# Kernel tuning notes

Hardware: AMD Instinct MI355X
Metric: run time of the kernel (lower is better)

Reference implementation:

```python
import jax, jax.numpy as jnp
import numpy as np

D = 1024       # d_model
H = 16         # num_heads
HD = D // H    # head_dim = 64
CS = 1024      # chunk_size
GS = 256       # global_context_size
CR = 4         # compression_ratio -> num_summary = CS // CR = 256
B = 2
S = 4096       # seq_len -> 4 chunks, no padding
NUM_CHUNKS = S // CS
SCALE = 1.0 / np.sqrt(HD)


def setup_inputs() -> dict:
    key = jax.random.key(0)
    ks = jax.random.split(key, 16)

    def lin(k, din, dout):
        kw, kb = jax.random.split(k)
        w = jax.random.normal(kw, (din, dout), jnp.float32) * (1.0 / np.sqrt(din))
        b = jnp.zeros((dout,), jnp.float32)
        return w, b

    cq_w, cq_b = lin(ks[0], D, D)
    ck_w, ck_b = lin(ks[1], D, D)
    cv_w, cv_b = lin(ks[2], D, D)
    co_w, co_b = lin(ks[3], D, D)
    qkv_w, qkv_b = lin(ks[4], D, 3 * D)
    lo_w, lo_b = lin(ks[5], D, D)
    summary_queries = jax.random.truncated_normal(ks[6], -2.0, 2.0, (1, CS // CR, D), jnp.float32) * 0.02
    x = jax.random.normal(ks[7], (B, S, D), jnp.float32)
    return {
        "x": x, "summary_queries": summary_queries,
        "cq_w": cq_w, "cq_b": cq_b, "ck_w": ck_w, "ck_b": ck_b,
        "cv_w": cv_w, "cv_b": cv_b, "co_w": co_w, "co_b": co_b,
        "qkv_w": qkv_w, "qkv_b": qkv_b, "lo_w": lo_w, "lo_b": lo_b,
    }


def _heads(t):
    # [B, L, D] -> [B, H, L, HD]
    b, l, _ = t.shape
    return jnp.transpose(t.reshape(b, l, H, HD), (0, 2, 1, 3))


def _unheads(t):
    # [B, H, L, HD] -> [B, L, D]
    b, _, l, _ = t.shape
    return jnp.transpose(t, (0, 2, 1, 3)).reshape(b, l, D)


def _compress_chunk(chunk, summary_queries, cq_w, cq_b, ck_w, ck_b, cv_w, cv_b, co_w, co_b):
    # chunk: [B, CS, D] -> [B, CS//CR, D] via learned-query cross-attention
    bsz = chunk.shape[0]
    sq = jnp.broadcast_to(summary_queries, (bsz, summary_queries.shape[1], D))
    q = _heads(sq @ cq_w + cq_b)        # [B, H, Ns, HD]
    k = _heads(chunk @ ck_w + ck_b)     # [B, H, CS, HD]
    v = _heads(chunk @ cv_w + cv_b)
    scores = jnp.einsum('bhqd,bhkd->bhqk', q, k) * SCALE
    weights = jax.nn.softmax(scores, axis=-1)
    out = _unheads(jnp.einsum('bhqk,bhkd->bhqd', weights, v))
    return out @ co_w + co_b


def _local_attention(chunk, gctx, qkv_w, qkv_b, lo_w, lo_b):
    # chunk: [B, CS, D], gctx: [B, G, D]
    g = gctx.shape[1]
    combined = jnp.concatenate([gctx, chunk], axis=1)   # [B, G+CS, D]
    cl = combined.shape[1]
    qkv = combined @ qkv_w + qkv_b
    q, k, v = jnp.split(qkv, 3, axis=-1)
    q, k, v = _heads(q), _heads(k), _heads(v)
    scores = jnp.einsum('bhqd,bhkd->bhqk', q, k) * SCALE
    # full visibility to global tokens, causal elsewhere
    idx = jnp.arange(cl)
    mask = (idx[None, :] < g) | (idx[None, :] <= idx[:, None])  # [cl, cl]
    scores = jnp.where(mask[None, None, :, :], scores, -1e9)
    weights = jax.nn.softmax(scores, axis=-1)
    attended = _unheads(jnp.einsum('bhqk,bhkd->bhqd', weights, v))
    attended = attended @ lo_w + lo_b
    return attended[:, g:] + chunk


def reference(x, summary_queries, cq_w, cq_b, ck_w, ck_b, cv_w, cv_b, co_w, co_b,
              qkv_w, qkv_b, lo_w, lo_b):
    comp = lambda c: _compress_chunk(c, summary_queries, cq_w, cq_b, ck_w, ck_b,
                                     cv_w, cv_b, co_w, co_b)
    # num_chunks > 1: global context = compression of first chunk (Ns == GS, no trunc)
    gctx = comp(x[:, :CS])
    outputs = []
    for i in range(NUM_CHUNKS):
        chunk = x[:, i * CS:(i + 1) * CS]
        chunk_out = _local_attention(chunk, gctx, qkv_w, qkv_b, lo_w, lo_b)
        outputs.append(chunk_out)
        if i < NUM_CHUNKS - 1:
            summ = comp(chunk_out)                       # [B, 256, D]
            gctx = jnp.concatenate([gctx, summ], axis=1)[:, -GS:]
    return jnp.concatenate(outputs, axis=1)  # [B, S, D]
```

## Files before the change

kernel.cpp:

```cpp
#include <hip/hip_runtime.h>

using bf16x8 = __attribute__((ext_vector_type(8))) short;
using f32x4  = __attribute__((ext_vector_type(4))) float;
using us4    = __attribute__((ext_vector_type(4))) unsigned short;

static __device__ __forceinline__ unsigned short f2bf(float x) {
  union { float f; unsigned u; } v; v.f = x;
  unsigned r = v.u + 0x7FFFu + ((v.u >> 16) & 1u);
  return (unsigned short)(r >> 16);
}
static __device__ __forceinline__ unsigned pack2bf(float a, float b) {
  return (unsigned)f2bf(a) | ((unsigned)f2bf(b) << 16);
}
static __device__ __forceinline__ void gload16(const unsigned short* g, unsigned short* lds_base) {
  __builtin_amdgcn_global_load_lds(
      (const __attribute__((address_space(1))) unsigned int*)g,
      (__attribute__((address_space(3))) unsigned int*)lds_base, 16, 0, 0);
}

#define SCALE_L2E 0.18033688011112042f
#define M0_L2E    14.426950408889634f

__global__ __launch_bounds__(256) void k_cvt(const float* __restrict__ in,
                                             unsigned short* __restrict__ out, int n4) {
  int i = blockIdx.x * 256 + threadIdx.x;
  if (i >= n4) return;
  float4 v = ((const float4*)in)[i];
  us4 o = { f2bf(v.x), f2bf(v.y), f2bf(v.z), f2bf(v.w) };
  ((us4*)out)[i] = o;
}

__global__ __launch_bounds__(256) void k_twt_all(
    const float* __restrict__ cq, const float* __restrict__ ck, const float* __restrict__ cv,
    const float* __restrict__ lo, const float* __restrict__ qkv,
    unsigned short* __restrict__ wqt, unsigned short* __restrict__ wkvt,
    unsigned short* __restrict__ wlot, unsigned short* __restrict__ wqkvt) {
  __shared__ float tile[32][33];
  int id = blockIdx.x;
  const float* W; unsigned short* Wt; int N;
  if (id < 1024)      { W = cq;  Wt = wqt;                N = 1024; }
  else if (id < 2048) { W = ck;  Wt = wkvt;               N = 1024; id -= 1024; }
  else if (id < 3072) { W = cv;  Wt = wkvt + 1024 * 1024; N = 1024; id -= 2048; }
  else if (id < 4096) { W = lo;  Wt = wlot;               N = 1024; id -= 3072; }
  else                { W = qkv; Wt = wqkvt;              N = 3072; id -= 4096; }
  int ntb = N >> 5;
  int nb = (id % ntb) * 32, kb = (id / ntb) * 32;
  int t = threadIdx.x;
  int k = t >> 3, n4 = (t & 7) << 2;
  float4 v = *(const float4*)&W[(size_t)(kb + k) * N + nb + n4];
  tile[k][n4] = v.x; tile[k][n4 + 1] = v.y; tile[k][n4 + 2] = v.z; tile[k][n4 + 3] = v.w;
  __syncthreads();
  int n = t >> 3, k4 = (t & 7) << 2;
  us4 o = { f2bf(tile[k4][n]), f2bf(tile[k4 + 1][n]), f2bf(tile[k4 + 2][n]), f2bf(tile[k4 + 3][n]) };
  *(us4*)&Wt[(size_t)(nb + n) * 1024 + kb + k4] = o;
}

__global__ __launch_bounds__(256) void k_bias2a(const float* __restrict__ qkv_w,
                                                const float* __restrict__ co_b,
                                                float* __restrict__ part) {
  int nb = blockIdx.x & 7, jb = blockIdx.x >> 3;
  int n = nb * 256 + threadIdx.x;
  float s = 0.f;
  int j0 = jb * 64;
#pragma unroll 4
  for (int j = j0; j < j0 + 64; ++j) s += co_b[j] * qkv_w[(size_t)j * 3072 + 1024 + n];
  part[jb * 2048 + n] = s;
}

__global__ __launch_bounds__(256) void k_bias2b(const float* __restrict__ part,
                                                const float* __restrict__ qkv_b,
                                                const float* __restrict__ ck_b,
                                                const float* __restrict__ cv_b,
                                                float* __restrict__ bias2,
                                                float* __restrict__ kvb,
                                                float* __restrict__ zbias) {
  int id = blockIdx.x, t = threadIdx.x;
  if (id < 8) {
    int n = id * 256 + t;
    float s = qkv_b[1024 + n];
#pragma unroll
    for (int jb = 0; jb < 16; ++jb) s += part[jb * 2048 + n];
    bias2[n] = s;
  } else {
    for (int j = t; j < 1024; j += 256) {
      kvb[j] = ck_b[j]; kvb[1024 + j] = cv_b[j]; zbias[j] = 0.f;
    }
  }
}

template <int BM, int NSTAGE = (BM == 256 ? 2 : 3)>
__global__ __launch_bounds__(BM * 2) void k_gemm(
    const unsigned short* __restrict__ A, long long bsA, int Lr,
    const unsigned short* __restrict__ Bt, const float* __restrict__ bias,
    unsigned short* __restrict__ outb, int Nout,
    unsigned short* __restrict__ outb2,
    unsigned short* __restrict__ outT, int Lv, int vt_col0,
    const float* __restrict__ resx, float* __restrict__ resout,
    unsigned short* __restrict__ rescob, int chunk,
    int N, int K) {
  constexpr int NWAVES = (BM * 2) / 64;
  constexpr int NA = BM / 16;
  constexpr int NINST = NA + 8;
  constexpr int NPW = NINST / NWAVES;
  static_assert(NPW * NWAVES == NINST, "staging split");
  constexpr int STRIDE = (BM + 128) * 32;
  __shared__ unsigned short Ls[NSTAGE * STRIDE];
  const int m0 = blockIdx.x * BM, n0 = blockIdx.y * 128;
  const int t = threadIdx.x, w = t >> 6, l = t & 63;
  const int wr = (BM == 64) ? 0 : (w >> 1);
  const int wc = (BM == 64) ? w : (w & 1);
  const int lg = l >> 4, lq = l & 15;
  const int batch = m0 / Lr, mrow = m0 % Lr;
  const int srow = l >> 2;
  const int scol = (((l & 3) ^ ((l >> 3) & 3)) << 3);
  const unsigned short* gp[NPW];
  int lofs[NPW];
#pragma unroll
  for (int jj = 0; jj < NPW; ++jj) {
    int j = w * NPW + jj;
    if (j < NA) {
      int r = mrow + j * 16 + srow;
      gp[jj] = A + (size_t)batch * (size_t)bsA + (size_t)r * K + scol;
      lofs[jj] = j * 512;
    } else {
      int r = n0 + (j - NA) * 16 + srow;
      gp[jj] = Bt + (size_t)r * K + scol;
      lofs[jj] = BM * 32 + (j - NA) * 512;
    }
  }
  const int lsw = (lg ^ ((lq >> 1) & 3)) * 8;
  const f32x4 fz = {0.f, 0.f, 0.f, 0.f};
  f32x4 acc[4][4];
#pragma unroll
  for (int i = 0; i < 4; ++i)
#pragma unroll
    for (int j = 0; j < 4; ++j) acc[i][j] = fz;
  const int nsteps = K >> 5;
#pragma unroll
  for (int st = 0; st < NSTAGE - 1; ++st) {
    if (st < nsteps) {
#pragma unroll
      for (int jj = 0; jj < NPW; ++jj) gload16(gp[jj] + (st << 5), &Ls[st * STRIDE + lofs[jj]]);
    }
  }
  int cur = 0;
  int nxt = (NSTAGE - 1) * STRIDE;
  for (int s = 0; s < nsteps; ++s) {
    if (s + NSTAGE - 1 < nsteps) {
      const int kk = (s + NSTAGE - 1) << 5;
#pragma unroll
      for (int jj = 0; jj < NPW; ++jj) gload16(gp[jj] + kk, &Ls[nxt + lofs[jj]]);
      asm volatile("s_waitcnt vmcnt(%0)" :: "n"((NSTAGE - 1) * NPW) : "memory");
    } else if (NSTAGE >= 3 && s + 1 < nsteps) {
      asm volatile("s_waitcnt vmcnt(%0)" :: "n"(NPW) : "memory");
    } else {
      asm volatile("s_waitcnt vmcnt(0)" ::: "memory");
    }
    __builtin_amdgcn_s_barrier();
    bf16x8 af[4], bg[4];
#pragma unroll
    for (int i = 0; i < 4; ++i) {
      af[i] = *(const bf16x8*)&Ls[cur + (wr * 64 + i * 16 + lq) * 32 + lsw];
      bg[i] = *(const bf16x8*)&Ls[cur + BM * 32 + (wc * 64 + i * 16 + lq) * 32 + lsw];
    }
#pragma unroll
    for (int i = 0; i < 4; ++i)
#pragma unroll
      for (int j = 0; j < 4; ++j)
        acc[i][j] = __builtin_amdgcn_mfma_f32_16x16x32_bf16(af[i], bg[j], acc[i][j], 0, 0, 0);
    __builtin_amdgcn_s_barrier();
    cur += STRIDE; if (cur == NSTAGE * STRIDE) cur = 0;
    nxt += STRIDE; if (nxt == NSTAGE * STRIDE) nxt = 0;
  }
  const int lr = lg << 2;
#pragma unroll
  for (int i = 0; i < 4; ++i) {
    const int rowb = m0 + wr * 64 + i * 16 + lr;
#pragma unroll
    for (int j = 0; j < 4; ++j) {
      const int col = n0 + wc * 64 + j * 16 + lq;
      const float bv = bias[col];
      float v0 = acc[i][j][0] + bv, v1 = acc[i][j][1] + bv;
      float v2 = acc[i][j][2] + bv, v3 = acc[i][j][3] + bv;
      if (outT && col >= vt_col0) {
        const int vc = col - vt_col0;
        const int hh = vc >> 6, dd = vc & 63;
        const int bb = rowb / Lr, key = rowb % Lr;
        us4 o = { f2bf(v0), f2bf(v1), f2bf(v2), f2bf(v3) };
        *(us4*)&outT[((size_t)((bb << 4) + hh) * 64 + dd) * Lv + key] = o;
      } else if (outb2 && col >= 1024) {
        const int c2 = col - 1024;
        outb2[(size_t)(rowb + 0) * 1024 + c2] = f2bf(v0);
        outb2[(size_t)(rowb + 1) * 1024 + c2] = f2bf(v1);
        outb2[(size_t)(rowb + 2) * 1024 + c2] = f2bf(v2);
        outb2[(size_t)(rowb + 3) * 1024 + c2] = f2bf(v3);
      } else if (resx) {
        const int bb = rowb / Lr, r = rowb % Lr;
        const size_t xo = ((size_t)(bb * 4096 + chunk * 1024 + r)) * 1024 + col;
        const size_t co = ((size_t)(bb * 1024 + r)) * 1024 + col;
        float r0 = v0 + resx[xo];
        float r1 = v1 + resx[xo + 1024];
        float r2 = v2 + resx[xo + 2048];
        float r3 = v3 + resx[xo + 3072];
        resout[xo] = r0; resout[xo + 1024] = r1;
        resout[xo + 2048] = r2; resout[xo + 3072] = r3;
        rescob[co] = f2bf(r0); rescob[co + 1024] = f2bf(r1);
        rescob[co + 2048] = f2bf(r2); rescob[co + 3072] = f2bf(r3);
      } else {
        outb[(size_t)(rowb + 0) * Nout + col] = f2bf(v0);
        outb[(size_t)(rowb + 1) * Nout + col] = f2bf(v1);
        outb[(size_t)(rowb + 2) * Nout + col] = f2bf(v2);
        outb[(size_t)(rowb + 3) * Nout + col] = f2bf(v3);
      }
    }
  }
}

template <int MODE>
__global__ __launch_bounds__(256) void k_fa(
    const unsigned short* __restrict__ Q, long long q_bs, int q_stride, int q_row0,
    const unsigned short* __restrict__ K, long long k_bs, int k_stride,
    const unsigned short* __restrict__ V, int Lk,
    unsigned short* __restrict__ O, int Lq_out,
    float* __restrict__ pl, float* __restrict__ pacc) {
  __shared__ unsigned short Ks[64 * 72];
  __shared__ unsigned short Vs[64 * 72];
  __shared__ unsigned short Ps[4 * 16 * 72];
  const int t = threadIdx.x, w = t >> 6, l = t & 63;
  const int lg = l >> 4, lq = l & 15;
  const int bh = blockIdx.x & 31;
  const int rest = blockIdx.x >> 5;
  const int b = bh >> 4, h = bh & 15;
  int qg, koff, ntiles;
  if (MODE == 1)      { qg = 15 - (rest & 15); koff = (rest >> 4) << 10; ntiles = qg + 1; }
  else if (MODE == 3) { qg = rest & 3;         koff = (rest >> 2) << 8;  ntiles = 4; }
  else                { qg = rest;             koff = 0;                 ntiles = 4; }
  const int qloc = qg * 64 + w * 16 + lq;
  const int qglob = q_row0 + (MODE == 1 ? koff : 0) + qloc;
  const unsigned short* qp = Q + (size_t)b * (size_t)q_bs + (size_t)qglob * q_stride + h * 64;
  bf16x8 qf0 = *(const bf16x8*)&qp[lg * 8];
  bf16x8 qf1 = *(const bf16x8*)&qp[32 + lg * 8];
  const f32x4 fz = {0.f, 0.f, 0.f, 0.f};
  const int pidx = (MODE == 2 ? 0 : (koff << 5)) + bh * (MODE == 3 ? 256 : 1024) + qloc;
  f32x4 acc0, acc1, acc2, acc3;
  float lbase = 0.f;
  if (MODE == 2) {
    lbase = pl[pidx];
    const float* pb = &pacc[(size_t)pidx * 64];
    float4 a0 = *(const float4*)&pb[0 * 16 + lg * 4];
    float4 a1 = *(const float4*)&pb[1 * 16 + lg * 4];
    float4 a2 = *(const float4*)&pb[2 * 16 + lg * 4];
    float4 a3 = *(const float4*)&pb[3 * 16 + lg * 4];
    acc0[0] = a0.x; acc0[1] = a0.y; acc0[2] = a0.z; acc0[3] = a0.w;
    acc1[0] = a1.x; acc1[1] = a1.y; acc1[2] = a1.z; acc1[3] = a1.w;
    acc2[0] = a2.x; acc2[1] = a2.y; acc2[2] = a2.z; acc2[3] = a2.w;
    acc3[0] = a3.x; acc3[1] = a3.y; acc3[2] = a3.z; acc3[3] = a3.w;
  } else {
    acc0 = fz; acc1 = fz; acc2 = fz; acc3 = fz;
  }
  float psum = 0.f;
  const int sr = t >> 2, sc = (t & 3) << 4;
  const unsigned short* kbp = K + (size_t)b * (size_t)k_bs + (size_t)koff * k_stride + h * 64;
  const unsigned short* vbp = V + (size_t)(((b << 4) + h) * 64) * Lk + koff;
  unsigned short* pw = &Ps[(w * 16 + lq) * 72];
  bf16x8 kr0, kr1, vr0, vr1;
  {
    const unsigned short* kp = kbp + (size_t)sr * k_stride + sc;
    kr0 = *(const bf16x8*)kp; kr1 = *(const bf16x8*)(kp + 8);
    const unsigned short* vp = vbp + (size_t)sr * Lk + sc;
    vr0 = *(const bf16x8*)vp; vr1 = *(const bf16x8*)(vp + 8);
  }
#define KFA_SM(Z, KH) do { \
    float e0_ = Z[0] * SCALE_L2E - M0_L2E; \
    float e1_ = Z[1] * SCALE_L2E - M0_L2E; \
    float e2_ = Z[2] * SCALE_L2E - M0_L2E; \
    float e3_ = Z[3] * SCALE_L2E - M0_L2E; \
    if (MODE == 1) { \
      int kg_ = k0 + (KH) * 16 + lg * 4; \
      if (kg_ + 0 > qloc) e0_ = -1e9f; \
      if (kg_ + 1 > qloc) e1_ = -1e9f; \
      if (kg_ + 2 > qloc) e2_ = -1e9f; \
      if (kg_ + 3 > qloc) e3_ = -1e9f; \
    } \
    float p0_ = exp2f(e0_), p1_ = exp2f(e1_), p2_ = exp2f(e2_), p3_ = exp2f(e3_); \
    psum += (p0_ + p1_) + (p2_ + p3_); \
    *(unsigned*)&pw[(KH) * 16 + lg * 4]     = pack2bf(p0_, p1_); \
    *(unsigned*)&pw[(KH) * 16 + lg * 4 + 2] = pack2bf(p2_, p3_); \
  } while (0)
#define KFA_MFMA(A_, B_, C_) __builtin_amdgcn_mfma_f32_16x16x32_bf16(A_, B_, C_, 0, 0, 0)
  for (int kt = 0; kt < ntiles; ++kt) {
    const int k0 = kt * 64;
    __syncthreads();
    *(bf16x8*)&Ks[sr * 72 + sc] = kr0; *(bf16x8*)&Ks[sr * 72 + sc + 8] = kr1;
    *(bf16x8*)&Vs[sr * 72 + sc] = vr0; *(bf16x8*)&Vs[sr * 72 + sc + 8] = vr1;
    __syncthreads();
    if (kt + 1 < ntiles) {
      const unsigned short* kp = kbp + (size_t)(k0 + 64 + sr) * k_stride + sc;
      kr0 = *(const bf16x8*)kp; kr1 = *(const bf16x8*)(kp + 8);
      const unsigned short* vp = vbp + (size_t)sr * Lk + k0 + 64 + sc;
      vr0 = *(const bf16x8*)vp; vr1 = *(const bf16x8*)(vp + 8);
    }
    f32x4 z0 = fz, z1 = fz, z2 = fz, z3 = fz;
    __builtin_amdgcn_s_setprio(1);
    z0 = KFA_MFMA(*(const bf16x8*)&Ks[(0 * 16 + lq) * 72 + lg * 8], qf0, z0);
    z1 = KFA_MFMA(*(const bf16x8*)&Ks[(1 * 16 + lq) * 72 + lg * 8], qf0, z1);
    z2 = KFA_MFMA(*(const bf16x8*)&Ks[(2 * 16 + lq) * 72 + lg * 8], qf0, z2);
    z3 = KFA_MFMA(*(const bf16x8*)&Ks[(3 * 16 + lq) * 72 + lg * 8], qf0, z3);
    z0 = KFA_MFMA(*(const bf16x8*)&Ks[(0 * 16 + lq) * 72 + 32 + lg * 8], qf1, z0);
    z1 = KFA_MFMA(*(const bf16x8*)&Ks[(1 * 16 + lq) * 72 + 32 + lg * 8], qf1, z1);
    z2 = KFA_MFMA(*(const bf16x8*)&Ks[(2 * 16 + lq) * 72 + 32 + lg * 8], qf1, z2);
    z3 = KFA_MFMA(*(const bf16x8*)&Ks[(3 * 16 + lq) * 72 + 32 + lg * 8], qf1, z3);
    __builtin_amdgcn_s_setprio(0);
    KFA_SM(z0, 0); KFA_SM(z1, 1); KFA_SM(z2, 2); KFA_SM(z3, 3);
    asm volatile("s_waitcnt lgkmcnt(0)" ::: "memory");
    __builtin_amdgcn_sched_barrier(0);
    bf16x8 pf0 = *(const bf16x8*)&pw[lg * 8];
    bf16x8 pf1 = *(const bf16x8*)&pw[32 + lg * 8];
    asm volatile("" ::: "memory");
    __builtin_amdgcn_sched_barrier(0);
    __builtin_amdgcn_s_setprio(1);
    acc0 = KFA_MFMA(*(const bf16x8*)&Vs[(0 * 16 + lq) * 72 + lg * 8], pf0, acc0);
    acc1 = KFA_MFMA(*(const bf16x8*)&Vs[(1 * 16 + lq) * 72 + lg * 8], pf0, acc1);
    acc2 = KFA_MFMA(*(const bf16x8*)&Vs[(2 * 16 + lq) * 72 + lg * 8], pf0, acc2);
    acc3 = KFA_MFMA(*(const bf16x8*)&Vs[(3 * 16 + lq) * 72 + lg * 8], pf0, acc3);
    acc0 = KFA_MFMA(*(const bf16x8*)&Vs[(0 * 16 + lq) * 72 + 32 + lg * 8], pf1, acc0);
    acc1 = KFA_MFMA(*(const bf16x8*)&Vs[(1 * 16 + lq) * 72 + 32 + lg * 8], pf1, acc1);
    acc2 = KFA_MFMA(*(const bf16x8*)&Vs[(2 * 16 + lq) * 72 + 32 + lg * 8], pf1, acc2);
    acc3 = KFA_MFMA(*(const bf16x8*)&Vs[(3 * 16 + lq) * 72 + 32 + lg * 8], pf1, acc3);
    __builtin_amdgcn_s_setprio(0);
  }
#undef KFA_SM
#undef KFA_MFMA
  psum += __shfl_xor(psum, 16);
  psum += __shfl_xor(psum, 32);
  if (MODE == 2) {
    float inv = 1.f / (lbase + psum);
    size_t ob = ((size_t)b * Lq_out + qloc) * 1024 + h * 64;
    us4 o0 = { f2bf(acc0[0] * inv), f2bf(acc0[1] * inv), f2bf(acc0[2] * inv), f2bf(acc0[3] * inv) };
    us4 o1 = { f2bf(acc1[0] * inv), f2bf(acc1[1] * inv), f2bf(acc1[2] * inv), f2bf(acc1[3] * inv) };
    us4 o2 = { f2bf(acc2[0] * inv), f2bf(acc2[1] * inv), f2bf(acc2[2] * inv), f2bf(acc2[3] * inv) };
    us4 o3 = { f2bf(acc3[0] * inv), f2bf(acc3[1] * inv), f2bf(acc3[2] * inv), f2bf(acc3[3] * inv) };
    *(us4*)&O[ob + 0 * 16 + lg * 4] = o0;
    *(us4*)&O[ob + 1 * 16 + lg * 4] = o1;
    *(us4*)&O[ob + 2 * 16 + lg * 4] = o2;
    *(us4*)&O[ob + 3 * 16 + lg * 4] = o3;
  } else {
    if (lg == 0) pl[pidx] = psum;
    float* pb = &pacc[(size_t)pidx * 64];
    *(float4*)&pb[0 * 16 + lg * 4] = make_float4(acc0[0], acc0[1], acc0[2], acc0[3]);
    *(float4*)&pb[1 * 16 + lg * 4] = make_float4(acc1[0], acc1[1], acc1[2], acc1[3]);
    *(float4*)&pb[2 * 16 + lg * 4] = make_float4(acc2[0], acc2[1], acc2[2], acc2[3]);
    *(float4*)&pb[3 * 16 + lg * 4] = make_float4(acc3[0], acc3[1], acc3[2], acc3[3]);
  }
}

__global__ __launch_bounds__(256) void k_fam(const float* __restrict__ pl0,
                                             const float* __restrict__ pacc0,
                                             unsigned short* __restrict__ attc) {
  int i = blockIdx.x * 256 + threadIdx.x;
  int row = i >> 4, d4 = (i & 15) << 2;
  float lsum = 0.f;
  float4 o = make_float4(0.f, 0.f, 0.f, 0.f);
#pragma unroll
  for (int s = 0; s < 4; ++s) {
    lsum += pl0[s * 8192 + row];
    float4 a = *(const float4*)&pacc0[((size_t)(s * 8192 + row)) * 64 + d4];
    o.x += a.x; o.y += a.y; o.z += a.z; o.w += a.w;
  }
  float inv = 1.f / lsum;
  int b = row >> 12, h = (row >> 8) & 15, q = row & 255;
  us4 ov = { f2bf(o.x * inv), f2bf(o.y * inv), f2bf(o.z * inv), f2bf(o.w * inv) };
  *(us4*)&attc[((size_t)(b * 256 + q)) * 1024 + h * 64 + d4] = ov;
}

extern "C" void kernel_launch(void* const* d_in, const int* in_sizes, int n_in,
                              void* d_out, int out_size, void* d_ws, size_t ws_size,
                              hipStream_t stream) {
  const float* x     = (const float*)d_in[0];
  const float* sq    = (const float*)d_in[1];
  const float* cq_w  = (const float*)d_in[2];
  const float* cq_b  = (const float*)d_in[3];
  const float* ck_w  = (const float*)d_in[4];
  const float* ck_b  = (const float*)d_in[5];
  const float* cv_w  = (const float*)d_in[6];
  const float* cv_b  = (const float*)d_in[7];
  const float* co_w  = (const float*)d_in[8];
  const float* co_b  = (const float*)d_in[9];
  const float* qkv_w = (const float*)d_in[10];
  const float* qkv_b = (const float*)d_in[11];
  const float* lo_w  = (const float*)d_in[12];
  const float* lo_b  = (const float*)d_in[13];
  float* out = (float*)d_out;

  char* ws = (char*)d_ws;
  size_t off = 0;
  auto alloc = [&](size_t bytes) -> void* {
    void* p = ws + off;
    off += (bytes + 255) & ~(size_t)255;
    return p;
  };
  unsigned short* xb    = (unsigned short*)alloc(16777216);
  unsigned short* sqb   = (unsigned short*)alloc(524288);
  unsigned short* cow16 = (unsigned short*)alloc(2097152);
  unsigned short* wqt   = (unsigned short*)alloc(2097152);
  unsigned short* wkvt  = (unsigned short*)alloc(4194304);
  unsigned short* wlot  = (unsigned short*)alloc(2097152);
  unsigned short* wqkvt = (unsigned short*)alloc(6291456);
  unsigned short* w2t   = (unsigned short*)alloc(4194304);
  float*          bias2 = (float*)alloc(8192);
  float*          kvb   = (float*)alloc(8192);
  float*          zbias = (float*)alloc(4096);
  float*          part  = (float*)alloc(131072);
  unsigned short* qs    = (unsigned short*)alloc(524288);
  unsigned short* qx    = (unsigned short*)alloc(16777216);
  unsigned short* kx    = (unsigned short*)alloc(16777216);
  unsigned short* vtx   = (unsigned short*)alloc(16777216);
  unsigned short* gk    = (unsigned short*)alloc(1048576);
  unsigned short* gvt   = (unsigned short*)alloc(1048576);
  unsigned short* kc    = (unsigned short*)alloc(4194304);
  unsigned short* vtc   = (unsigned short*)alloc(4194304);
  unsigned short* attc  = (unsigned short*)alloc(1048576);
  unsigned short* attl  = (unsigned short*)alloc(4194304);
  unsigned short* cob   = (unsigned short*)alloc(4194304);
  float*          plb   = (float*)alloc(524288);
  float*          pacc  = (float*)alloc(33554432);
  float*          pl0   = (float*)alloc(131072);
  float*          pacc0 = (float*)alloc(8388608);

  k_cvt<<<8192, 256, 0, stream>>>(x, xb, 2097152);
  k_cvt<<<256, 256, 0, stream>>>(sq, sqb, 65536);
  k_cvt<<<1024, 256, 0, stream>>>(co_w, cow16, 262144);
  k_twt_all<<<7168, 256, 0, stream>>>(cq_w, ck_w, cv_w, lo_w, qkv_w, wqt, wkvt, wlot, wqkvt);
  k_bias2a<<<128, 256, 0, stream>>>(qkv_w, co_b, part);
  k_bias2b<<<9, 256, 0, stream>>>(part, qkv_b, ck_b, cv_b, bias2, kvb, zbias);
  k_gemm<64><<<dim3(4, 8), 128, 0, stream>>>(sqb, 0, 256, wqt, cq_b, qs, 1024, nullptr,
                                             nullptr, 0, 0, nullptr, nullptr, nullptr, 0, 1024, 1024);
  k_gemm<128><<<dim3(16, 8), 256, 0, stream>>>(wqkvt + 1024 * 1024, 0, 2048, cow16, zbias,
                                               w2t, 1024, nullptr, nullptr, 0, 0,
                                               nullptr, nullptr, nullptr, 0, 1024, 1024);
  k_gemm<256><<<dim3(32, 24), 512, 0, stream>>>(xb, 4096LL * 1024, 4096, wqkvt, qkv_b,
                                                qx, 1024, kx, vtx, 4096, 2048,
                                                nullptr, nullptr, nullptr, 0, 3072, 1024);
  k_fa<1><<<2048, 256, 0, stream>>>(qx, 4096LL * 1024, 1024, 0,
                                    kx, 4096LL * 1024, 1024,
                                    vtx, 4096, nullptr, 0, plb, pacc);

  auto comp = [&](const unsigned short* inA, long long bsA) {
    k_gemm<64><<<dim3(32, 16), 128, 0, stream>>>(inA, bsA, 1024, wkvt, kvb,
                                                 kc, 1024, nullptr, vtc, 1024, 1024,
                                                 nullptr, nullptr, nullptr, 0, 2048, 1024);
    k_fa<3><<<512, 256, 0, stream>>>(qs, 0LL, 1024, 0,
                                     kc, 1024LL * 1024, 1024,
                                     vtc, 1024, nullptr, 0, pl0, pacc0);
    k_fam<<<512, 256, 0, stream>>>(pl0, pacc0, attc);
    k_gemm<64><<<dim3(8, 16), 128, 0, stream>>>(attc, 256LL * 1024, 256, w2t, bias2,
                                                gk, 1024, nullptr, gvt, 256, 1024,
                                                nullptr, nullptr, nullptr, 0, 2048, 1024);
  };

  comp(xb, 4096LL * 1024);
  for (int i = 0; i < 4; ++i) {
    k_fa<2><<<512, 256, 0, stream>>>(qx, 4096LL * 1024, 1024, i * 1024,
                                     gk, 256LL * 1024, 1024,
                                     gvt, 256, attl, 1024,
                                     plb + (size_t)i * 32768, pacc + (size_t)i * 32768 * 64);
    k_gemm<64><<<dim3(32, 8), 128, 0, stream>>>(attl, 1024LL * 1024, 1024, wlot, lo_b,
                                                nullptr, 1024, nullptr, nullptr, 0, 0,
                                                x, out, cob, i, 1024, 1024);
    if (i < 3) comp(cob, 1024LL * 1024);
  }
}
```

Measured before the change: 477.8 us.

## Drop split-K compression attention, double-buffer FA tiles, fuse conversion kernels

The compression attention no longer splits the 1024 keys into four partial blocks followed by a merge kernel. A new MODE 0 processes all 16 key tiles in a single pass over 128 blocks and writes normalized bf16 output directly. This removes the k_fam launch and the fp32 partial buffers, at the cost of less parallelism per launch. The flash-attention loop now double-buffers the K/V LDS tiles, dropping one __syncthreads per iteration. The three fp32-to-bf16 conversion launches are also merged into one.

```diff
diff --git a/kernel.cpp b/kernel.cpp
--- a/kernel.cpp
+++ b/kernel.cpp
@@ -21,10 +21,17 @@
 #define SCALE_L2E 0.18033688011112042f
 #define M0_L2E    14.426950408889634f
 
-__global__ __launch_bounds__(256) void k_cvt(const float* __restrict__ in,
-                                             unsigned short* __restrict__ out, int n4) {
-  int i = blockIdx.x * 256 + threadIdx.x;
-  if (i >= n4) return;
+__global__ __launch_bounds__(256) void k_cvt3(const float* __restrict__ x,
+                                              const float* __restrict__ sq,
+                                              const float* __restrict__ cw,
+                                              unsigned short* __restrict__ xb,
+                                              unsigned short* __restrict__ sqb,
+                                              unsigned short* __restrict__ cwb) {
+  int id = blockIdx.x;
+  const float* in; unsigned short* out; int i;
+  if (id < 8192)      { in = x;  out = xb;  i = id * 256 + threadIdx.x; }
+  else if (id < 8448) { in = sq; out = sqb; i = (id - 8192) * 256 + threadIdx.x; }
+  else                { in = cw; out = cwb; i = (id - 8448) * 256 + threadIdx.x; }
   float4 v = ((const float4*)in)[i];
   us4 o = { f2bf(v.x), f2bf(v.y), f2bf(v.z), f2bf(v.w) };
   ((us4*)out)[i] = o;
@@ -222,9 +229,9 @@
     const unsigned short* __restrict__ K, long long k_bs, int k_stride,
     const unsigned short* __restrict__ V, int Lk,
     unsigned short* __restrict__ O, int Lq_out,
-    float* __restrict__ pl, float* __restrict__ pacc) {
-  __shared__ unsigned short Ks[64 * 72];
-  __shared__ unsigned short Vs[64 * 72];
+    float* __restrict__ pl, float* __restrict__ pacc, int Lkeys) {
+  __shared__ unsigned short Ks[2][64 * 72];
+  __shared__ unsigned short Vs[2][64 * 72];
   __shared__ unsigned short Ps[4 * 16 * 72];
   const int t = threadIdx.x, w = t >> 6, l = t & 63;
   const int lg = l >> 4, lq = l & 15;
@@ -232,16 +239,15 @@
   const int rest = blockIdx.x >> 5;
   const int b = bh >> 4, h = bh & 15;
   int qg, koff, ntiles;
-  if (MODE == 1)      { qg = 15 - (rest & 15); koff = (rest >> 4) << 10; ntiles = qg + 1; }
-  else if (MODE == 3) { qg = rest & 3;         koff = (rest >> 2) << 8;  ntiles = 4; }
-  else                { qg = rest;             koff = 0;                 ntiles = 4; }
+  if (MODE == 1) { qg = 15 - (rest & 15); koff = (rest >> 4) << 10; ntiles = qg + 1; }
+  else           { qg = rest;             koff = 0;                 ntiles = Lkeys >> 6; }
   const int qloc = qg * 64 + w * 16 + lq;
   const int qglob = q_row0 + (MODE == 1 ? koff : 0) + qloc;
   const unsigned short* qp = Q + (size_t)b * (size_t)q_bs + (size_t)qglob * q_stride + h * 64;
   bf16x8 qf0 = *(const bf16x8*)&qp[lg * 8];
   bf16x8 qf1 = *(const bf16x8*)&qp[32 + lg * 8];
   const f32x4 fz = {0.f, 0.f, 0.f, 0.f};
-  const int pidx = (MODE == 2 ? 0 : (koff << 5)) + bh * (MODE == 3 ? 256 : 1024) + qloc;
+  const int pidx = (MODE == 1 ? (koff << 5) : 0) + bh * 1024 + qloc;
   f32x4 acc0, acc1, acc2, acc3;
   float lbase = 0.f;
   if (MODE == 2) {
@@ -290,9 +296,9 @@
 #define KFA_MFMA(A_, B_, C_) __builtin_amdgcn_mfma_f32_16x16x32_bf16(A_, B_, C_, 0, 0, 0)
   for (int kt = 0; kt < ntiles; ++kt) {
     const int k0 = kt * 64;
-    __syncthreads();
-    *(bf16x8*)&Ks[sr * 72 + sc] = kr0; *(bf16x8*)&Ks[sr * 72 + sc + 8] = kr1;
-    *(bf16x8*)&Vs[sr * 72 + sc] = vr0; *(bf16x8*)&Vs[sr * 72 + sc + 8] = vr1;
+    const int p = kt & 1;
+    *(bf16x8*)&Ks[p][sr * 72 + sc] = kr0; *(bf16x8*)&Ks[p][sr * 72 + sc + 8] = kr1;
+    *(bf16x8*)&Vs[p][sr * 72 + sc] = vr0; *(bf16x8*)&Vs[p][sr * 72 + sc + 8] = vr1;
     __syncthreads();
     if (kt + 1 < ntiles) {
       const unsigned short* kp = kbp + (size_t)(k0 + 64 + sr) * k_stride + sc;
@@ -302,14 +308,14 @@
     }
     f32x4 z0 = fz, z1 = fz, z2 = fz, z3 = fz;
     __builtin_amdgcn_s_setprio(1);
-    z0 = KFA_MFMA(*(const bf16x8*)&Ks[(0 * 16 + lq) * 72 + lg * 8], qf0, z0);
-    z1 = KFA_MFMA(*(const bf16x8*)&Ks[(1 * 16 + lq) * 72 + lg * 8], qf0, z1);
-    z2 = KFA_MFMA(*(const bf16x8*)&Ks[(2 * 16 + lq) * 72 + lg * 8], qf0, z2);
-    z3 = KFA_MFMA(*(const bf16x8*)&Ks[(3 * 16 + lq) * 72 + lg * 8], qf0, z3);
-    z0 = KFA_MFMA(*(const bf16x8*)&Ks[(0 * 16 + lq) * 72 + 32 + lg * 8], qf1, z0);
-    z1 = KFA_MFMA(*(const bf16x8*)&Ks[(1 * 16 + lq) * 72 + 32 + lg * 8], qf1, z1);
-    z2 = KFA_MFMA(*(const bf16x8*)&Ks[(2 * 16 + lq) * 72 + 32 + lg * 8], qf1, z2);
-    z3 = KFA_MFMA(*(const bf16x8*)&Ks[(3 * 16 + lq) * 72 + 32 + lg * 8], qf1, z3);
+    z0 = KFA_MFMA(*(const bf16x8*)&Ks[p][(0 * 16 + lq) * 72 + lg * 8], qf0, z0);
+    z1 = KFA_MFMA(*(const bf16x8*)&Ks[p][(1 * 16 + lq) * 72 + lg * 8], qf0, z1);
+    z2 = KFA_MFMA(*(const bf16x8*)&Ks[p][(2 * 16 + lq) * 72 + lg * 8], qf0, z2);
+    z3 = KFA_MFMA(*(const bf16x8*)&Ks[p][(3 * 16 + lq) * 72 + lg * 8], qf0, z3);
+    z0 = KFA_MFMA(*(const bf16x8*)&Ks[p][(0 * 16 + lq) * 72 + 32 + lg * 8], qf1, z0);
+    z1 = KFA_MFMA(*(const bf16x8*)&Ks[p][(1 * 16 + lq) * 72 + 32 + lg * 8], qf1, z1);
+    z2 = KFA_MFMA(*(const bf16x8*)&Ks[p][(2 * 16 + lq) * 72 + 32 + lg * 8], qf1, z2);
+    z3 = KFA_MFMA(*(const bf16x8*)&Ks[p][(3 * 16 + lq) * 72 + 32 + lg * 8], qf1, z3);
     __builtin_amdgcn_s_setprio(0);
     KFA_SM(z0, 0); KFA_SM(z1, 1); KFA_SM(z2, 2); KFA_SM(z3, 3);
     asm volatile("s_waitcnt lgkmcnt(0)" ::: "memory");
@@ -319,21 +325,28 @@
     asm volatile("" ::: "memory");
     __builtin_amdgcn_sched_barrier(0);
     __builtin_amdgcn_s_setprio(1);
-    acc0 = KFA_MFMA(*(const bf16x8*)&Vs[(0 * 16 + lq) * 72 + lg * 8], pf0, acc0);
-    acc1 = KFA_MFMA(*(const bf16x8*)&Vs[(1 * 16 + lq) * 72 + lg * 8], pf0, acc1);
-    acc2 = KFA_MFMA(*(const bf16x8*)&Vs[(2 * 16 + lq) * 72 + lg * 8], pf0, acc2);
-    acc3 = KFA_MFMA(*(const bf16x8*)&Vs[(3 * 16 + lq) * 72 + lg * 8], pf0, acc3);
-    acc0 = KFA_MFMA(*(const bf16x8*)&Vs[(0 * 16 + lq) * 72 + 32 + lg * 8], pf1, acc0);
-    acc1 = KFA_MFMA(*(const bf16x8*)&Vs[(1 * 16 + lq) * 72 + 32 + lg * 8], pf1, acc1);
-    acc2 = KFA_MFMA(*(const bf16x8*)&Vs[(2 * 16 + lq) * 72 + 32 + lg * 8], pf1, acc2);
-    acc3 = KFA_MFMA(*(const bf16x8*)&Vs[(3 * 16 + lq) * 72 + 32 + lg * 8], pf1, acc3);
+    acc0 = KFA_MFMA(*(const bf16x8*)&Vs[p][(0 * 16 + lq) * 72 + lg * 8], pf0, acc0);
+    acc1 = KFA_MFMA(*(const bf16x8*)&Vs[p][(1 * 16 + lq) * 72 + lg * 8], pf0, acc1);
+    acc2 = KFA_MFMA(*(const bf16x8*)&Vs[p][(2 * 16 + lq) * 72 + lg * 8], pf0, acc2);
+    acc3 = KFA_MFMA(*(const bf16x8*)&Vs[p][(3 * 16 + lq) * 72 + lg * 8], pf0, acc3);
+    acc0 = KFA_MFMA(*(const bf16x8*)&Vs[p][(0 * 16 + lq) * 72 + 32 + lg * 8], pf1, acc0);
+    acc1 = KFA_MFMA(*(const bf16x8*)&Vs[p][(1 * 16 + lq) * 72 + 32 + lg * 8], pf1, acc1);
+    acc2 = KFA_MFMA(*(const bf16x8*)&Vs[p][(2 * 16 + lq) * 72 + 32 + lg * 8], pf1, acc2);
+    acc3 = KFA_MFMA(*(const bf16x8*)&Vs[p][(3 * 16 + lq) * 72 + 32 + lg * 8], pf1, acc3);
     __builtin_amdgcn_s_setprio(0);
   }
 #undef KFA_SM
 #undef KFA_MFMA
   psum += __shfl_xor(psum, 16);
   psum += __shfl_xor(psum, 32);
-  if (MODE == 2) {
+  if (MODE == 1) {
+    if (lg == 0) pl[pidx] = psum;
+    float* pb = &pacc[(size_t)pidx * 64];
+    *(float4*)&pb[0 * 16 + lg * 4] = make_float4(acc0[0], acc0[1], acc0[2], acc0[3]);
+    *(float4*)&pb[1 * 16 + lg * 4] = make_float4(acc1[0], acc1[1], acc1[2], acc1[3]);
+    *(float4*)&pb[2 * 16 + lg * 4] = make_float4(acc2[0], acc2[1], acc2[2], acc2[3]);
+    *(float4*)&pb[3 * 16 + lg * 4] = make_float4(acc3[0], acc3[1], acc3[2], acc3[3]);
+  } else {
     float inv = 1.f / (lbase + psum);
     size_t ob = ((size_t)b * Lq_out + qloc) * 1024 + h * 64;
     us4 o0 = { f2bf(acc0[0] * inv), f2bf(acc0[1] * inv), f2bf(acc0[2] * inv), f2bf(acc0[3] * inv) };
@@ -344,33 +357,7 @@
     *(us4*)&O[ob + 1 * 16 + lg * 4] = o1;
     *(us4*)&O[ob + 2 * 16 + lg * 4] = o2;
     *(us4*)&O[ob + 3 * 16 + lg * 4] = o3;
-  } else {
-    if (lg == 0) pl[pidx] = psum;
-    float* pb = &pacc[(size_t)pidx * 64];
-    *(float4*)&pb[0 * 16 + lg * 4] = make_float4(acc0[0], acc0[1], acc0[2], acc0[3]);
-    *(float4*)&pb[1 * 16 + lg * 4] = make_float4(acc1[0], acc1[1], acc1[2], acc1[3]);
-    *(float4*)&pb[2 * 16 + lg * 4] = make_float4(acc2[0], acc2[1], acc2[2], acc2[3]);
-    *(float4*)&pb[3 * 16 + lg * 4] = make_float4(acc3[0], acc3[1], acc3[2], acc3[3]);
-  }
-}
-
-__global__ __launch_bounds__(256) void k_fam(const float* __restrict__ pl0,
-                                             const float* __restrict__ pacc0,
-                                             unsigned short* __restrict__ attc) {
-  int i = blockIdx.x * 256 + threadIdx.x;
-  int row = i >> 4, d4 = (i & 15) << 2;
-  float lsum = 0.f;
-  float4 o = make_float4(0.f, 0.f, 0.f, 0.f);
-#pragma unroll
-  for (int s = 0; s < 4; ++s) {
-    lsum += pl0[s * 8192 + row];
-    float4 a = *(const float4*)&pacc0[((size_t)(s * 8192 + row)) * 64 + d4];
-    o.x += a.x; o.y += a.y; o.z += a.z; o.w += a.w;
-  }
-  float inv = 1.f / lsum;
-  int b = row >> 12, h = (row >> 8) & 15, q = row & 255;
-  us4 ov = { f2bf(o.x * inv), f2bf(o.y * inv), f2bf(o.z * inv), f2bf(o.w * inv) };
-  *(us4*)&attc[((size_t)(b * 256 + q)) * 1024 + h * 64 + d4] = ov;
+  }
 }
 
 extern "C" void kernel_launch(void* const* d_in, const int* in_sizes, int n_in,
@@ -424,12 +411,8 @@
   unsigned short* cob   = (unsigned short*)alloc(4194304);
   float*          plb   = (float*)alloc(524288);
   float*          pacc  = (float*)alloc(33554432);
-  float*          pl0   = (float*)alloc(131072);
-  float*          pacc0 = (float*)alloc(8388608);
-
-  k_cvt<<<8192, 256, 0, stream>>>(x, xb, 2097152);
-  k_cvt<<<256, 256, 0, stream>>>(sq, sqb, 65536);
-  k_cvt<<<1024, 256, 0, stream>>>(co_w, cow16, 262144);
+
+  k_cvt3<<<9472, 256, 0, stream>>>(x, sq, co_w, xb, sqb, cow16);
   k_twt_all<<<7168, 256, 0, stream>>>(cq_w, ck_w, cv_w, lo_w, qkv_w, wqt, wkvt, wlot, wqkvt);
   k_bias2a<<<128, 256, 0, stream>>>(qkv_w, co_b, part);
   k_bias2b<<<9, 256, 0, stream>>>(part, qkv_b, ck_b, cv_b, bias2, kvb, zbias);
@@ -443,16 +426,15 @@
                                                 nullptr, nullptr, nullptr, 0, 3072, 1024);
   k_fa<1><<<2048, 256, 0, stream>>>(qx, 4096LL * 1024, 1024, 0,
                                     kx, 4096LL * 1024, 1024,
-                                    vtx, 4096, nullptr, 0, plb, pacc);
+                                    vtx, 4096, nullptr, 0, plb, pacc, 1024);
 
   auto comp = [&](const unsigned short* inA, long long bsA) {
     k_gemm<64><<<dim3(32, 16), 128, 0, stream>>>(inA, bsA, 1024, wkvt, kvb,
                                                  kc, 1024, nullptr, vtc, 1024, 1024,
                                                  nullptr, nullptr, nullptr, 0, 2048, 1024);
-    k_fa<3><<<512, 256, 0, stream>>>(qs, 0LL, 1024, 0,
+    k_fa<0><<<128, 256, 0, stream>>>(qs, 0LL, 1024, 0,
                                      kc, 1024LL * 1024, 1024,
-                                     vtc, 1024, nullptr, 0, pl0, pacc0);
-    k_fam<<<512, 256, 0, stream>>>(pl0, pacc0, attc);
+                                     vtc, 1024, attc, 256, nullptr, nullptr, 1024);
     k_gemm<64><<<dim3(8, 16), 128, 0, stream>>>(attc, 256LL * 1024, 256, w2t, bias2,
                                                 gk, 1024, nullptr, gvt, 256, 1024,
                                                 nullptr, nullptr, nullptr, 0, 2048, 1024);
@@ -463,7 +445,7 @@
     k_fa<2><<<512, 256, 0, stream>>>(qx, 4096LL * 1024, 1024, i * 1024,
                                      gk, 256LL * 1024, 1024,
                                      gvt, 256, attl, 1024,
-                                     plb + (size_t)i * 32768, pacc + (size_t)i * 32768 * 64);
+                                     plb + (size_t)i * 32768, pacc + (size_t)i * 32768 * 64, 256);
     k_gemm<64><<<dim3(32, 8), 128, 0, stream>>>(attl, 1024LL * 1024, 1024, wlot, lo_b,
                                                 nullptr, 1024, nullptr, nullptr, 0, 0,
                                                 x, out, cob, i, 1024, 1024);
```

New measurement: 491.3 us. 1.03x slower.

## Merge prep kernels and fuse split-K merge into compression attention via counters

Applied to the files above, without the earlier changes.

Folds the three fp32-to-bf16 conversions, the weight transposes and the first bias reduction into one k_prep launch. It also removes the k_fam merge kernel: each MODE 3 attention block bumps an atomic counter, and the last of the four key-split blocks reduces the partial sums and writes the normalized output. This cuts several launches and launch gaps per compression step. The cost is a memset, threadfences and atomics, plus serial merge work in the last-arriving block.

```diff
diff --git a/kernel.cpp b/kernel.cpp
--- a/kernel.cpp
+++ b/kernel.cpp
@@ -21,50 +21,54 @@
 #define SCALE_L2E 0.18033688011112042f
 #define M0_L2E    14.426950408889634f
 
-__global__ __launch_bounds__(256) void k_cvt(const float* __restrict__ in,
-                                             unsigned short* __restrict__ out, int n4) {
-  int i = blockIdx.x * 256 + threadIdx.x;
-  if (i >= n4) return;
-  float4 v = ((const float4*)in)[i];
-  us4 o = { f2bf(v.x), f2bf(v.y), f2bf(v.z), f2bf(v.w) };
-  ((us4*)out)[i] = o;
-}
-
-__global__ __launch_bounds__(256) void k_twt_all(
+__global__ __launch_bounds__(256) void k_prep(
+    const float* __restrict__ x, const float* __restrict__ sq, const float* __restrict__ cw,
+    unsigned short* __restrict__ xb, unsigned short* __restrict__ sqb,
+    unsigned short* __restrict__ cwb,
     const float* __restrict__ cq, const float* __restrict__ ck, const float* __restrict__ cv,
     const float* __restrict__ lo, const float* __restrict__ qkv,
     unsigned short* __restrict__ wqt, unsigned short* __restrict__ wkvt,
-    unsigned short* __restrict__ wlot, unsigned short* __restrict__ wqkvt) {
+    unsigned short* __restrict__ wlot, unsigned short* __restrict__ wqkvt,
+    const float* __restrict__ qkv_w, const float* __restrict__ co_b,
+    float* __restrict__ part) {
   __shared__ float tile[32][33];
   int id = blockIdx.x;
-  const float* W; unsigned short* Wt; int N;
-  if (id < 1024)      { W = cq;  Wt = wqt;                N = 1024; }
-  else if (id < 2048) { W = ck;  Wt = wkvt;               N = 1024; id -= 1024; }
-  else if (id < 3072) { W = cv;  Wt = wkvt + 1024 * 1024; N = 1024; id -= 2048; }
-  else if (id < 4096) { W = lo;  Wt = wlot;               N = 1024; id -= 3072; }
-  else                { W = qkv; Wt = wqkvt;              N = 3072; id -= 4096; }
-  int ntb = N >> 5;
-  int nb = (id % ntb) * 32, kb = (id / ntb) * 32;
-  int t = threadIdx.x;
-  int k = t >> 3, n4 = (t & 7) << 2;
-  float4 v = *(const float4*)&W[(size_t)(kb + k) * N + nb + n4];
-  tile[k][n4] = v.x; tile[k][n4 + 1] = v.y; tile[k][n4 + 2] = v.z; tile[k][n4 + 3] = v.w;
-  __syncthreads();
-  int n = t >> 3, k4 = (t & 7) << 2;
-  us4 o = { f2bf(tile[k4][n]), f2bf(tile[k4 + 1][n]), f2bf(tile[k4 + 2][n]), f2bf(tile[k4 + 3][n]) };
-  *(us4*)&Wt[(size_t)(nb + n) * 1024 + kb + k4] = o;
-}
-
-__global__ __launch_bounds__(256) void k_bias2a(const float* __restrict__ qkv_w,
-                                                const float* __restrict__ co_b,
-                                                float* __restrict__ part) {
-  int nb = blockIdx.x & 7, jb = blockIdx.x >> 3;
-  int n = nb * 256 + threadIdx.x;
-  float s = 0.f;
-  int j0 = jb * 64;
+  const int t = threadIdx.x;
+  if (id < 9472) {
+    const float* in; unsigned short* out; int i;
+    if (id < 8192)      { in = x;  out = xb;  i = id * 256 + t; }
+    else if (id < 8448) { in = sq; out = sqb; i = (id - 8192) * 256 + t; }
+    else                { in = cw; out = cwb; i = (id - 8448) * 256 + t; }
+    float4 v = ((const float4*)in)[i];
+    us4 o = { f2bf(v.x), f2bf(v.y), f2bf(v.z), f2bf(v.w) };
+    ((us4*)out)[i] = o;
+  } else if (id < 16640) {
+    id -= 9472;
+    const float* W; unsigned short* Wt; int N;
+    if (id < 1024)      { W = cq;  Wt = wqt;                N = 1024; }
+    else if (id < 2048) { W = ck;  Wt = wkvt;               N = 1024; id -= 1024; }
+    else if (id < 3072) { W = cv;  Wt = wkvt + 1024 * 1024; N = 1024; id -= 2048; }
+    else if (id < 4096) { W = lo;  Wt = wlot;               N = 1024; id -= 3072; }
+    else                { W = qkv; Wt = wqkvt;              N = 3072; id -= 4096; }
+    int ntb = N >> 5;
+    int nb = (id % ntb) * 32, kb = (id / ntb) * 32;
+    int k = t >> 3, n4 = (t & 7) << 2;
+    float4 v = *(const float4*)&W[(size_t)(kb + k) * N + nb + n4];
+    tile[k][n4] = v.x; tile[k][n4 + 1] = v.y; tile[k][n4 + 2] = v.z; tile[k][n4 + 3] = v.w;
+    __syncthreads();
+    int n = t >> 3, k4 = (t & 7) << 2;
+    us4 o = { f2bf(tile[k4][n]), f2bf(tile[k4 + 1][n]), f2bf(tile[k4 + 2][n]), f2bf(tile[k4 + 3][n]) };
+    *(us4*)&Wt[(size_t)(nb + n) * 1024 + kb + k4] = o;
+  } else {
+    id -= 16640;
+    int nb = id & 7, jb = id >> 3;
+    int n = nb * 256 + t;
+    float s = 0.f;
+    int j0 = jb * 64;
 #pragma unroll 4
-  for (int j = j0; j < j0 + 64; ++j) s += co_b[j] * qkv_w[(size_t)j * 3072 + 1024 + n];
-  part[jb * 2048 + n] = s;
+    for (int j = j0; j < j0 + 64; ++j) s += co_b[j] * qkv_w[(size_t)j * 3072 + 1024 + n];
+    part[jb * 2048 + n] = s;
+  }
 }
 
 __global__ __launch_bounds__(256) void k_bias2b(const float* __restrict__ part,
@@ -222,10 +226,11 @@
     const unsigned short* __restrict__ K, long long k_bs, int k_stride,
     const unsigned short* __restrict__ V, int Lk,
     unsigned short* __restrict__ O, int Lq_out,
-    float* __restrict__ pl, float* __restrict__ pacc) {
+    float* __restrict__ pl, float* __restrict__ pacc, int* __restrict__ cnt) {
   __shared__ unsigned short Ks[64 * 72];
   __shared__ unsigned short Vs[64 * 72];
   __shared__ unsigned short Ps[4 * 16 * 72];
+  __shared__ int mflag;
   const int t = threadIdx.x, w = t >> 6, l = t & 63;
   const int lg = l >> 4, lq = l & 15;
   const int bh = blockIdx.x & 31;
@@ -351,26 +356,31 @@
     *(float4*)&pb[1 * 16 + lg * 4] = make_float4(acc1[0], acc1[1], acc1[2], acc1[3]);
     *(float4*)&pb[2 * 16 + lg * 4] = make_float4(acc2[0], acc2[1], acc2[2], acc2[3]);
     *(float4*)&pb[3 * 16 + lg * 4] = make_float4(acc3[0], acc3[1], acc3[2], acc3[3]);
-  }
-}
-
-__global__ __launch_bounds__(256) void k_fam(const float* __restrict__ pl0,
-                                             const float* __restrict__ pacc0,
-                                             unsigned short* __restrict__ attc) {
-  int i = blockIdx.x * 256 + threadIdx.x;
-  int row = i >> 4, d4 = (i & 15) << 2;
-  float lsum = 0.f;
-  float4 o = make_float4(0.f, 0.f, 0.f, 0.f);
-#pragma unroll
-  for (int s = 0; s < 4; ++s) {
-    lsum += pl0[s * 8192 + row];
-    float4 a = *(const float4*)&pacc0[((size_t)(s * 8192 + row)) * 64 + d4];
-    o.x += a.x; o.y += a.y; o.z += a.z; o.w += a.w;
-  }
-  float inv = 1.f / lsum;
-  int b = row >> 12, h = (row >> 8) & 15, q = row & 255;
-  us4 ov = { f2bf(o.x * inv), f2bf(o.y * inv), f2bf(o.z * inv), f2bf(o.w * inv) };
-  *(us4*)&attc[((size_t)(b * 256 + q)) * 1024 + h * 64 + d4] = ov;
+    if (MODE == 3) {
+      __threadfence();
+      if (t == 0) mflag = atomicAdd(&cnt[bh * 4 + qg], 1);
+      __syncthreads();
+      if (mflag == 3) {
+        __threadfence();
+        for (int it = t; it < 1024; it += 256) {
+          const int r = it >> 4, d4 = (it & 15) << 2;
+          const int row = bh * 256 + qg * 64 + r;
+          float lsum = 0.f;
+          float4 o = make_float4(0.f, 0.f, 0.f, 0.f);
+#pragma unroll
+          for (int s = 0; s < 4; ++s) {
+            lsum += pl[s * 8192 + row];
+            float4 a = *(const float4*)&pacc[((size_t)(s * 8192 + row)) * 64 + d4];
+            o.x += a.x; o.y += a.y; o.z += a.z; o.w += a.w;
+          }
+          float inv = 1.f / lsum;
+          const int q = qg * 64 + r;
+          us4 ov = { f2bf(o.x * inv), f2bf(o.y * inv), f2bf(o.z * inv), f2bf(o.w * inv) };
+          *(us4*)&O[((size_t)(b * 256 + q)) * 1024 + h * 64 + d4] = ov;
+        }
+      }
+    }
+  }
 }
 
 extern "C" void kernel_launch(void* const* d_in, const int* in_sizes, int n_in,
@@ -426,12 +436,14 @@
   float*          pacc  = (float*)alloc(33554432);
   float*          pl0   = (float*)alloc(131072);
   float*          pacc0 = (float*)alloc(8388608);
-
-  k_cvt<<<8192, 256, 0, stream>>>(x, xb, 2097152);
-  k_cvt<<<256, 256, 0, stream>>>(sq, sqb, 65536);
-  k_cvt<<<1024, 256, 0, stream>>>(co_w, cow16, 262144);
-  k_twt_all<<<7168, 256, 0, stream>>>(cq_w, ck_w, cv_w, lo_w, qkv_w, wqt, wkvt, wlot, wqkvt);
-  k_bias2a<<<128, 256, 0, stream>>>(qkv_w, co_b, part);
+  int*            cnt   = (int*)alloc(4 * 128 * sizeof(int));
+
+  hipMemsetAsync(cnt, 0, 4 * 128 * sizeof(int), stream);
+
+  k_prep<<<16768, 256, 0, stream>>>(x, sq, co_w, xb, sqb, cow16,
+                                    cq_w, ck_w, cv_w, lo_w, qkv_w,
+                                    wqt, wkvt, wlot, wqkvt,
+                                    qkv_w, co_b, part);
   k_bias2b<<<9, 256, 0, stream>>>(part, qkv_b, ck_b, cv_b, bias2, kvb, zbias);
   k_gemm<64><<<dim3(4, 8), 128, 0, stream>>>(sqb, 0, 256, wqt, cq_b, qs, 1024, nullptr,
                                              nullptr, 0, 0, nullptr, nullptr, nullptr, 0, 1024, 1024);
@@ -443,16 +455,18 @@
                                                 nullptr, nullptr, nullptr, 0, 3072, 1024);
   k_fa<1><<<2048, 256, 0, stream>>>(qx, 4096LL * 1024, 1024, 0,
                                     kx, 4096LL * 1024, 1024,
-                                    vtx, 4096, nullptr, 0, plb, pacc);
-
+                                    vtx, 4096, nullptr, 0, plb, pacc, nullptr);
+
+  int compCall = 0;
   auto comp = [&](const unsigned short* inA, long long bsA) {
     k_gemm<64><<<dim3(32, 16), 128, 0, stream>>>(inA, bsA, 1024, wkvt, kvb,
                                                  kc, 1024, nullptr, vtc, 1024, 1024,
                                                  nullptr, nullptr, nullptr, 0, 2048, 1024);
     k_fa<3><<<512, 256, 0, stream>>>(qs, 0LL, 1024, 0,
                                      kc, 1024LL * 1024, 1024,
-                                     vtc, 1024, nullptr, 0, pl0, pacc0);
-    k_fam<<<512, 256, 0, stream>>>(pl0, pacc0, attc);
+                                     vtc, 1024, attc, 256, pl0, pacc0,
+                                     cnt + compCall * 128);
+    ++compCall;
     k_gemm<64><<<dim3(8, 16), 128, 0, stream>>>(attc, 256LL * 1024, 256, w2t, bias2,
                                                 gk, 1024, nullptr, gvt, 256, 1024,
                                                 nullptr, nullptr, nullptr, 0, 2048, 1024);
@@ -463,7 +477,8 @@
     k_fa<2><<<512, 256, 0, stream>>>(qx, 4096LL * 1024, 1024, i * 1024,
                                      gk, 256LL * 1024, 1024,
                                      gvt, 256, attl, 1024,
-                                     plb + (size_t)i * 32768, pacc + (size_t)i * 32768 * 64);
+                                     plb + (size_t)i * 32768, pacc + (size_t)i * 32768 * 64,
+                                     nullptr);
     k_gemm<64><<<dim3(32, 8), 128, 0, stream>>>(attl, 1024LL * 1024, 1024, wlot, lo_b,
                                                 nullptr, 1024, nullptr, nullptr, 0, 0,
                                                 x, out, cob, i, 1024, 1024);
```

Result: slower. 723.8 us (+51.5%).
